# Optimization experiments

Hardware: AMD Instinct MI355X
Metric: run time of the kernel (lower is better)

## Reference

```python
import jax, jax.numpy as jnp
import numpy as np

D_MODEL, D_K, D_V, H = 1024, 64, 64, 16


def setup_inputs() -> dict:
    key = jax.random.key(0)
    ks = jax.random.split(key, 11)
    b, nq, nk = 2, 2048, 2048
    queries = jax.random.normal(ks[0], (b, nq, D_MODEL), dtype=jnp.float32)
    keys = jax.random.normal(ks[1], (b, nk, D_MODEL), dtype=jnp.float32)
    values = jax.random.normal(ks[2], (b, nk, D_MODEL), dtype=jnp.float32)
    def xavier(k, shape):
        fan_in, fan_out = shape[1], shape[0]
        lim = np.sqrt(6.0 / (fan_in + fan_out)).astype(np.float32)
        return jax.random.uniform(k, shape, jnp.float32, -lim, lim)
    # torch Linear weight shape: (out_features, in_features)
    Wq = xavier(ks[3], (H * D_K, D_MODEL)); bq = jnp.zeros((H * D_K,), jnp.float32)
    Wk = xavier(ks[4], (H * D_K, D_MODEL)); bk = jnp.zeros((H * D_K,), jnp.float32)
    Wv = xavier(ks[5], (H * D_V, D_MODEL)); bv = jnp.zeros((H * D_V,), jnp.float32)
    Wo = xavier(ks[6], (D_MODEL, H * D_V)); bo = jnp.zeros((D_MODEL,), jnp.float32)
    return {"queries": queries, "keys": keys, "values": values,
            "Wq": Wq, "bq": bq, "Wk": Wk, "bk": bk,
            "Wv": Wv, "bv": bv, "Wo": Wo, "bo": bo}


def reference(queries, keys, values, Wq, bq, Wk, bk, Wv, bv, Wo, bo):
    b, nq, _ = queries.shape
    nk = keys.shape[1]
    scale = 1.0 / np.sqrt(D_K).astype(np.float32)
    # projections -> (b, h, n, d)
    q = (queries @ Wq.T + bq).reshape(b, nq, H, D_K).transpose(0, 2, 1, 3)
    k = (keys @ Wk.T + bk).reshape(b, nk, H, D_K).transpose(0, 2, 1, 3)
    v = (values @ Wv.T + bv).reshape(b, nk, H, D_V).transpose(0, 2, 1, 3)
    att = jnp.einsum('bhqd,bhkd->bhqk', q, k) * scale  # (b,h,nq,nk)
    att = jax.nn.softmax(att, axis=-1)
    out = jnp.einsum('bhqk,bhkd->bhqd', att, v)        # (b,h,nq,dv)
    out = out.transpose(0, 2, 1, 3).reshape(b, nq, H * D_V)
    return out @ Wo.T + bo
```

## Files before the change

### kernel.cpp

```cpp
#include <hip/hip_runtime.h>
#include <stdint.h>

typedef __bf16 v8bf __attribute__((ext_vector_type(8)));
typedef float  v4f  __attribute__((ext_vector_type(4)));

#define QSCALE 0.18033688011112042f

typedef __attribute__((address_space(3))) void lds_vp;
typedef const __attribute__((address_space(1))) void gbl_vp;
__device__ __forceinline__ void gl_lds16(const __bf16* g, __bf16* l) {
    __builtin_amdgcn_global_load_lds((gbl_vp*)g, (lds_vp*)l, 16, 0, 0);
}

__device__ __forceinline__ v8bf cvt8(const float* __restrict__ p) {
    float4 x = *reinterpret_cast<const float4*>(p);
    float4 y = *reinterpret_cast<const float4*>(p + 4);
    v8bf r;
    r[0] = (__bf16)x.x; r[1] = (__bf16)x.y; r[2] = (__bf16)x.z; r[3] = (__bf16)x.w;
    r[4] = (__bf16)y.x; r[5] = (__bf16)y.y; r[6] = (__bf16)y.z; r[7] = (__bf16)y.w;
    return r;
}

__global__ __launch_bounds__(256) void cvt_w(
    const float* __restrict__ w0, const float* __restrict__ w1,
    const float* __restrict__ w2, const float* __restrict__ w3,
    __bf16* __restrict__ o0, __bf16* __restrict__ o1,
    __bf16* __restrict__ o2, __bf16* __restrict__ o3)
{
    const float* src; __bf16* dst;
    switch (blockIdx.y) {
        case 0: src = w0; dst = o0; break;
        case 1: src = w1; dst = o1; break;
        case 2: src = w2; dst = o2; break;
        default: src = w3; dst = o3; break;
    }
    size_t i = ((size_t)blockIdx.x * 256 + threadIdx.x) * 8;
    *reinterpret_cast<v8bf*>(dst + i) = cvt8(src + i);
}

__global__ __launch_bounds__(256) void cvt_in(
    const float* __restrict__ i0, const float* __restrict__ i1,
    const float* __restrict__ i2,
    __bf16* __restrict__ o0, __bf16* __restrict__ o1, __bf16* __restrict__ o2)
{
    const float* src; __bf16* dst;
    switch (blockIdx.y) {
        case 0: src = i0; dst = o0; break;
        case 1: src = i1; dst = o1; break;
        default: src = i2; dst = o2; break;
    }
    size_t i = ((size_t)blockIdx.x * 256 + threadIdx.x) * 8;
    *reinterpret_cast<v8bf*>(dst + i) = cvt8(src + i);
}

template<int MT>
__device__ __forceinline__ void gemm_body(
    const __bf16* __restrict__ A, const __bf16* __restrict__ W,
    const float* __restrict__ bias, void* __restrict__ outp,
    int mode, float oscale, int bx, int by)
{
    constexpr int K = 1024, N = 1024;
    constexpr int WM = MT / 32;
    constexpr int AI = MT / 32;
    constexpr int BI = 4;
    __shared__ __align__(16) __bf16 As[MT * 64];
    __shared__ __align__(16) __bf16 Bs[128 * 64];

    const int lane = threadIdx.x & 63;
    const int wave = threadIdx.x >> 6;
    const int quad = lane >> 4;
    const int l15  = lane & 15;
    const int m_base = bx * MT;
    const int n_base = by * 128;
    const int wm = (wave & 1) * (MT / 2);
    const int wn = (wave >> 1) * 64;

    int arow[AI], acol[AI], brow[BI], bcol[BI];
    #pragma unroll
    for (int i = 0; i < AI; ++i) {
        int L = (i * 4 + wave) * 64 + lane;
        int r = L >> 3, s = L & 7;
        arow[i] = r; acol[i] = (s ^ (r & 7)) * 8;
    }
    #pragma unroll
    for (int i = 0; i < BI; ++i) {
        int L = (i * 4 + wave) * 64 + lane;
        int r = L >> 3, s = L & 7;
        brow[i] = r; bcol[i] = (s ^ (r & 7)) * 8;
    }

    v4f acc[WM][4];
    #pragma unroll
    for (int fa = 0; fa < WM; ++fa)
        #pragma unroll
        for (int fb = 0; fb < 4; ++fb) { v4f z = {0.f,0.f,0.f,0.f}; acc[fa][fb] = z; }

    for (int kb = 0; kb < K; kb += 64) {
        #pragma unroll
        for (int i = 0; i < AI; ++i)
            gl_lds16(A + (size_t)(m_base + arow[i]) * K + kb + acol[i],
                     &As[(size_t)(i * 4 + wave) * 512]);
        #pragma unroll
        for (int i = 0; i < BI; ++i)
            gl_lds16(W + (size_t)(n_base + brow[i]) * K + kb + bcol[i],
                     &Bs[(size_t)(i * 4 + wave) * 512]);
        __syncthreads();
        #pragma unroll
        for (int ks = 0; ks < 2; ++ks) {
            v8bf af[WM], bf[4];
            #pragma unroll
            for (int f = 0; f < WM; ++f) {
                const int R = wm + f * 16 + l15;
                const int slot = (ks * 4 + quad) ^ (R & 7);
                af[f] = *reinterpret_cast<const v8bf*>(&As[R * 64 + slot * 8]);
            }
            #pragma unroll
            for (int f = 0; f < 4; ++f) {
                const int R = wn + f * 16 + l15;
                const int slot = (ks * 4 + quad) ^ (R & 7);
                bf[f] = *reinterpret_cast<const v8bf*>(&Bs[R * 64 + slot * 8]);
            }
            #pragma unroll
            for (int fa = 0; fa < WM; ++fa)
                #pragma unroll
                for (int fb = 0; fb < 4; ++fb)
                    acc[fa][fb] = __builtin_amdgcn_mfma_f32_16x16x32_bf16(
                        af[fa], bf[fb], acc[fa][fb], 0, 0, 0);
        }
        __syncthreads();
    }

    #pragma unroll
    for (int fa = 0; fa < WM; ++fa)
        #pragma unroll
        for (int fb = 0; fb < 4; ++fb) {
            const int nc = n_base + wn + fb * 16 + l15;
            const float bval = bias[nc];
            #pragma unroll
            for (int r = 0; r < 4; ++r) {
                const int m = m_base + wm + fa * 16 + quad * 4 + r;
                const float v = (acc[fa][fb][r] + bval) * oscale;
                if (mode == 2) {
                    ((float*)outp)[(size_t)m * N + nc] = v;
                } else {
                    int b = m >> 11, n = m & 2047, h = nc >> 6, d = nc & 63;
                    size_t off = (mode == 0)
                        ? ((size_t)(b * 16 + h) * 2048 + n) * 64 + d
                        : ((size_t)(b * 16 + h) * 64 + d) * 2048 + n;
                    ((__bf16*)outp)[off] = (__bf16)v;
                }
            }
        }
}

__global__ __launch_bounds__(256) void qkv_gemm(
    const __bf16* __restrict__ Aq, const __bf16* __restrict__ Ak,
    const __bf16* __restrict__ Av,
    const __bf16* __restrict__ Wq, const __bf16* __restrict__ Wk,
    const __bf16* __restrict__ Wv,
    const float* __restrict__ bq, const float* __restrict__ bk,
    const float* __restrict__ bv,
    __bf16* __restrict__ Qo, __bf16* __restrict__ Ko, __bf16* __restrict__ Vo)
{
    const __bf16 *A, *W; const float* bias; __bf16* outp; float oscale; int mode;
    switch (blockIdx.z) {
        case 0:  A = Aq; W = Wq; bias = bq; outp = Qo; oscale = QSCALE; mode = 0; break;
        case 1:  A = Ak; W = Wk; bias = bk; outp = Ko; oscale = 1.0f;   mode = 0; break;
        default: A = Av; W = Wv; bias = bv; outp = Vo; oscale = 1.0f;   mode = 1; break;
    }
    gemm_body<128>(A, W, bias, outp, mode, oscale, blockIdx.x, blockIdx.y);
}

__global__ __launch_bounds__(256) void out_gemm(
    const __bf16* __restrict__ A, const __bf16* __restrict__ W,
    const float* __restrict__ bias, float* __restrict__ outp)
{
    gemm_body<64>(A, W, bias, outp, 2, 1.0f, blockIdx.x, blockIdx.y);
}

__global__ __launch_bounds__(256) void attn_kernel(
    const __bf16* __restrict__ Q, const __bf16* __restrict__ Kb_,
    const __bf16* __restrict__ Vt, __bf16* __restrict__ O)
{
    __shared__ __align__(16) __bf16 Ks[64 * 64];
    __shared__ __align__(16) __bf16 Vs[64 * 64];
    __shared__ __align__(16) __bf16 p_lds[4][2][16][72];

    const int lane = threadIdx.x & 63;
    const int wave = threadIdx.x >> 6;
    const int quad = lane >> 4;
    const int l15  = lane & 15;
    const int qt = blockIdx.x;
    const int bh = blockIdx.y;
    const int b  = bh >> 4, h = bh & 15;

    const __bf16* Qh = Q   + (size_t)bh * 2048 * 64;
    const __bf16* Kh = Kb_ + (size_t)bh * 2048 * 64;
    const __bf16* Vh = Vt  + (size_t)bh * 64 * 2048;

    int srow[2], scol[2];
    #pragma unroll
    for (int i = 0; i < 2; ++i) {
        int L = (i * 4 + wave) * 64 + lane;
        int r = L >> 3, s = L & 7;
        srow[i] = r; scol[i] = (s ^ (r & 7)) * 8;
    }

    v8bf qf[2][2];
    #pragma unroll
    for (int s = 0; s < 2; ++s)
        #pragma unroll
        for (int ks = 0; ks < 2; ++ks)
            qf[s][ks] = *reinterpret_cast<const v8bf*>(
                Qh + (size_t)(qt * 128 + wave * 32 + s * 16 + l15) * 64 + ks * 32 + quad * 8);

    v4f o_acc[2][4];
    #pragma unroll
    for (int s = 0; s < 2; ++s)
        #pragma unroll
        for (int c = 0; c < 4; ++c) { v4f z = {0.f,0.f,0.f,0.f}; o_acc[s][c] = z; }
    float l_r[2][4];
    #pragma unroll
    for (int s = 0; s < 2; ++s)
        #pragma unroll
        for (int r = 0; r < 4; ++r) l_r[s][r] = 0.f;

    for (int kt = 0; kt < 32; ++kt) {
        #pragma unroll
        for (int i = 0; i < 2; ++i) {
            gl_lds16(Kh + (size_t)(kt * 64 + srow[i]) * 64 + scol[i],
                     &Ks[(size_t)(i * 4 + wave) * 512]);
            gl_lds16(Vh + (size_t)srow[i] * 2048 + kt * 64 + scol[i],
                     &Vs[(size_t)(i * 4 + wave) * 512]);
        }
        __syncthreads();

        v4f s_t[2][4];
        #pragma unroll
        for (int s = 0; s < 2; ++s)
            #pragma unroll
            for (int c = 0; c < 4; ++c) { v4f z = {0.f,0.f,0.f,0.f}; s_t[s][c] = z; }
        #pragma unroll
        for (int ks = 0; ks < 2; ++ks) {
            v8bf kf[4];
            #pragma unroll
            for (int c = 0; c < 4; ++c) {
                const int R = c * 16 + l15;
                const int slot = (ks * 4 + quad) ^ (R & 7);
                kf[c] = *reinterpret_cast<const v8bf*>(&Ks[R * 64 + slot * 8]);
            }
            #pragma unroll
            for (int c = 0; c < 4; ++c) {
                s_t[0][c] = __builtin_amdgcn_mfma_f32_16x16x32_bf16(qf[0][ks], kf[c], s_t[0][c], 0, 0, 0);
                s_t[1][c] = __builtin_amdgcn_mfma_f32_16x16x32_bf16(qf[1][ks], kf[c], s_t[1][c], 0, 0, 0);
            }
        }

        #pragma unroll
        for (int s = 0; s < 2; ++s)
            #pragma unroll
            for (int r = 0; r < 4; ++r) {
                const float p0 = __builtin_exp2f(s_t[s][0][r]);
                const float p1 = __builtin_exp2f(s_t[s][1][r]);
                const float p2 = __builtin_exp2f(s_t[s][2][r]);
                const float p3 = __builtin_exp2f(s_t[s][3][r]);
                l_r[s][r] += (p0 + p1) + (p2 + p3);
                p_lds[wave][s][quad * 4 + r][0 * 16 + l15] = (__bf16)p0;
                p_lds[wave][s][quad * 4 + r][1 * 16 + l15] = (__bf16)p1;
                p_lds[wave][s][quad * 4 + r][2 * 16 + l15] = (__bf16)p2;
                p_lds[wave][s][quad * 4 + r][3 * 16 + l15] = (__bf16)p3;
            }

        #pragma unroll
        for (int ks = 0; ks < 2; ++ks) {
            v8bf vf[4];
            #pragma unroll
            for (int c = 0; c < 4; ++c) {
                const int R = c * 16 + l15;
                const int slot = (ks * 4 + quad) ^ (R & 7);
                vf[c] = *reinterpret_cast<const v8bf*>(&Vs[R * 64 + slot * 8]);
            }
            #pragma unroll
            for (int s = 0; s < 2; ++s) {
                v8bf pf = *reinterpret_cast<const v8bf*>(&p_lds[wave][s][l15][ks * 32 + quad * 8]);
                #pragma unroll
                for (int c = 0; c < 4; ++c)
                    o_acc[s][c] = __builtin_amdgcn_mfma_f32_16x16x32_bf16(pf, vf[c], o_acc[s][c], 0, 0, 0);
            }
        }
        __syncthreads();
    }

    #pragma unroll
    for (int s = 0; s < 2; ++s)
        #pragma unroll
        for (int r = 0; r < 4; ++r) {
            float l = l_r[s][r];
            #pragma unroll
            for (int off = 1; off < 16; off <<= 1)
                l += __shfl_xor(l, off, 16);
            const float inv_l = 1.0f / l;
            const int qr = qt * 128 + wave * 32 + s * 16 + quad * 4 + r;
            #pragma unroll
            for (int c = 0; c < 4; ++c) {
                const int col = h * 64 + c * 16 + l15;
                O[(size_t)(b * 2048 + qr) * 1024 + col] = (__bf16)(o_acc[s][c][r] * inv_l);
            }
        }
}

extern "C" void kernel_launch(void* const* d_in, const int* in_sizes, int n_in,
                              void* d_out, int out_size, void* d_ws, size_t ws_size,
                              hipStream_t stream) {
    const float* q_in = (const float*)d_in[0];
    const float* k_in = (const float*)d_in[1];
    const float* v_in = (const float*)d_in[2];
    const float* Wq = (const float*)d_in[3];
    const float* bq = (const float*)d_in[4];
    const float* Wk = (const float*)d_in[5];
    const float* bk = (const float*)d_in[6];
    const float* Wv = (const float*)d_in[7];
    const float* bv = (const float*)d_in[8];
    const float* Wo = (const float*)d_in[9];
    const float* bo = (const float*)d_in[10];
    float* out = (float*)d_out;

    __bf16* ws  = (__bf16*)d_ws;
    __bf16* Abq = ws;
    __bf16* Abk = Abq + 4194304;
    __bf16* Abv = Abk + 4194304;
    __bf16* Qb  = Abv + 4194304;
    __bf16* Kb  = Qb  + 4194304;
    __bf16* Vb  = Kb  + 4194304;
    __bf16* Wqb = Vb  + 4194304;
    __bf16* Wkb = Wqb + 1048576;
    __bf16* Wvb = Wkb + 1048576;
    __bf16* Wob = Wvb + 1048576;
    __bf16* Ob  = Abq;

    cvt_w<<<dim3(512, 4), 256, 0, stream>>>(Wq, Wk, Wv, Wo, Wqb, Wkb, Wvb, Wob);
    cvt_in<<<dim3(2048, 3), 256, 0, stream>>>(q_in, k_in, v_in, Abq, Abk, Abv);

    qkv_gemm<<<dim3(32, 8, 3), 256, 0, stream>>>(
        Abq, Abk, Abv, Wqb, Wkb, Wvb, bq, bk, bv, Qb, Kb, Vb);

    attn_kernel<<<dim3(16, 32), 256, 0, stream>>>(Qb, Kb, Vb, Ob);

    out_gemm<<<dim3(64, 8), 256, 0, stream>>>(Ob, Wob, bo, out);
}
```

Baseline: 255.5 us.

## Double-buffer LDS tiles in GEMMs and attention, retile and remap block order

Result: no change. 254.7 us (-0.3%).

```diff
diff --git a/kernel.cpp b/kernel.cpp
--- a/kernel.cpp
+++ b/kernel.cpp
@@ -53,93 +53,101 @@
     *reinterpret_cast<v8bf*>(dst + i) = cvt8(src + i);
 }
 
-template<int MT>
 __device__ __forceinline__ void gemm_body(
     const __bf16* __restrict__ A, const __bf16* __restrict__ W,
     const float* __restrict__ bias, void* __restrict__ outp,
     int mode, float oscale, int bx, int by)
 {
     constexpr int K = 1024, N = 1024;
-    constexpr int WM = MT / 32;
-    constexpr int AI = MT / 32;
-    constexpr int BI = 4;
-    __shared__ __align__(16) __bf16 As[MT * 64];
-    __shared__ __align__(16) __bf16 Bs[128 * 64];
+    __shared__ __align__(16) __bf16 As[2][128 * 64];
+    __shared__ __align__(16) __bf16 Bs[2][64 * 64];
 
     const int lane = threadIdx.x & 63;
     const int wave = threadIdx.x >> 6;
     const int quad = lane >> 4;
     const int l15  = lane & 15;
-    const int m_base = bx * MT;
-    const int n_base = by * 128;
-    const int wm = (wave & 1) * (MT / 2);
-    const int wn = (wave >> 1) * 64;
-
-    int arow[AI], acol[AI], brow[BI], bcol[BI];
-    #pragma unroll
-    for (int i = 0; i < AI; ++i) {
+    const int m_base = bx * 128;
+    const int n_base = by * 64;
+    const int wm = (wave & 1) * 64;
+    const int wn = (wave >> 1) * 32;
+
+    int arow[4], acol[4], brow[2], bcol[2];
+    #pragma unroll
+    for (int i = 0; i < 4; ++i) {
         int L = (i * 4 + wave) * 64 + lane;
         int r = L >> 3, s = L & 7;
         arow[i] = r; acol[i] = (s ^ (r & 7)) * 8;
     }
     #pragma unroll
-    for (int i = 0; i < BI; ++i) {
+    for (int i = 0; i < 2; ++i) {
         int L = (i * 4 + wave) * 64 + lane;
         int r = L >> 3, s = L & 7;
         brow[i] = r; bcol[i] = (s ^ (r & 7)) * 8;
     }
 
-    v4f acc[WM][4];
-    #pragma unroll
-    for (int fa = 0; fa < WM; ++fa)
-        #pragma unroll
-        for (int fb = 0; fb < 4; ++fb) { v4f z = {0.f,0.f,0.f,0.f}; acc[fa][fb] = z; }
-
-    for (int kb = 0; kb < K; kb += 64) {
-        #pragma unroll
-        for (int i = 0; i < AI; ++i)
-            gl_lds16(A + (size_t)(m_base + arow[i]) * K + kb + acol[i],
-                     &As[(size_t)(i * 4 + wave) * 512]);
-        #pragma unroll
-        for (int i = 0; i < BI; ++i)
-            gl_lds16(W + (size_t)(n_base + brow[i]) * K + kb + bcol[i],
-                     &Bs[(size_t)(i * 4 + wave) * 512]);
-        __syncthreads();
+    v4f acc[4][2];
+    #pragma unroll
+    for (int f = 0; f < 4; ++f)
+        #pragma unroll
+        for (int g = 0; g < 2; ++g) { v4f z = {0.f,0.f,0.f,0.f}; acc[f][g] = z; }
+
+    #pragma unroll
+    for (int i = 0; i < 4; ++i)
+        gl_lds16(A + (size_t)(m_base + arow[i]) * K + acol[i],
+                 &As[0][(i * 4 + wave) * 512]);
+    #pragma unroll
+    for (int i = 0; i < 2; ++i)
+        gl_lds16(W + (size_t)(n_base + brow[i]) * K + bcol[i],
+                 &Bs[0][(i * 4 + wave) * 512]);
+    __syncthreads();
+
+    for (int it = 0; it < 16; ++it) {
+        const int cur = it & 1, nxt = cur ^ 1;
+        const int kn = ((it + 1) & 15) * 64;
+        #pragma unroll
+        for (int i = 0; i < 4; ++i)
+            gl_lds16(A + (size_t)(m_base + arow[i]) * K + kn + acol[i],
+                     &As[nxt][(i * 4 + wave) * 512]);
+        #pragma unroll
+        for (int i = 0; i < 2; ++i)
+            gl_lds16(W + (size_t)(n_base + brow[i]) * K + kn + bcol[i],
+                     &Bs[nxt][(i * 4 + wave) * 512]);
+
         #pragma unroll
         for (int ks = 0; ks < 2; ++ks) {
-            v8bf af[WM], bf[4];
-            #pragma unroll
-            for (int f = 0; f < WM; ++f) {
+            v8bf af[4], bf[2];
+            #pragma unroll
+            for (int f = 0; f < 4; ++f) {
                 const int R = wm + f * 16 + l15;
                 const int slot = (ks * 4 + quad) ^ (R & 7);
-                af[f] = *reinterpret_cast<const v8bf*>(&As[R * 64 + slot * 8]);
-            }
-            #pragma unroll
-            for (int f = 0; f < 4; ++f) {
-                const int R = wn + f * 16 + l15;
+                af[f] = *reinterpret_cast<const v8bf*>(&As[cur][R * 64 + slot * 8]);
+            }
+            #pragma unroll
+            for (int g = 0; g < 2; ++g) {
+                const int R = wn + g * 16 + l15;
                 const int slot = (ks * 4 + quad) ^ (R & 7);
-                bf[f] = *reinterpret_cast<const v8bf*>(&Bs[R * 64 + slot * 8]);
-            }
-            #pragma unroll
-            for (int fa = 0; fa < WM; ++fa)
+                bf[g] = *reinterpret_cast<const v8bf*>(&Bs[cur][R * 64 + slot * 8]);
+            }
+            #pragma unroll
+            for (int f = 0; f < 4; ++f)
                 #pragma unroll
-                for (int fb = 0; fb < 4; ++fb)
-                    acc[fa][fb] = __builtin_amdgcn_mfma_f32_16x16x32_bf16(
-                        af[fa], bf[fb], acc[fa][fb], 0, 0, 0);
+                for (int g = 0; g < 2; ++g)
+                    acc[f][g] = __builtin_amdgcn_mfma_f32_16x16x32_bf16(
+                        af[f], bf[g], acc[f][g], 0, 0, 0);
         }
         __syncthreads();
     }
 
     #pragma unroll
-    for (int fa = 0; fa < WM; ++fa)
-        #pragma unroll
-        for (int fb = 0; fb < 4; ++fb) {
-            const int nc = n_base + wn + fb * 16 + l15;
+    for (int f = 0; f < 4; ++f)
+        #pragma unroll
+        for (int g = 0; g < 2; ++g) {
+            const int nc = n_base + wn + g * 16 + l15;
             const float bval = bias[nc];
             #pragma unroll
             for (int r = 0; r < 4; ++r) {
-                const int m = m_base + wm + fa * 16 + quad * 4 + r;
-                const float v = (acc[fa][fb][r] + bval) * oscale;
+                const int m = m_base + wm + f * 16 + quad * 4 + r;
+                const float v = (acc[f][g][r] + bval) * oscale;
                 if (mode == 2) {
                     ((float*)outp)[(size_t)m * N + nc] = v;
                 } else {
@@ -162,36 +170,43 @@
     const float* __restrict__ bv,
     __bf16* __restrict__ Qo, __bf16* __restrict__ Ko, __bf16* __restrict__ Vo)
 {
+    const int id = blockIdx.x;
+    const int by = id & 15;
+    const int bx = (id >> 4) & 31;
+    const int z  = id >> 9;
+
     const __bf16 *A, *W; const float* bias; __bf16* outp; float oscale; int mode;
-    switch (blockIdx.z) {
+    switch (z) {
         case 0:  A = Aq; W = Wq; bias = bq; outp = Qo; oscale = QSCALE; mode = 0; break;
         case 1:  A = Ak; W = Wk; bias = bk; outp = Ko; oscale = 1.0f;   mode = 0; break;
         default: A = Av; W = Wv; bias = bv; outp = Vo; oscale = 1.0f;   mode = 1; break;
     }
-    gemm_body<128>(A, W, bias, outp, mode, oscale, blockIdx.x, blockIdx.y);
+    gemm_body(A, W, bias, outp, mode, oscale, bx, by);
 }
 
 __global__ __launch_bounds__(256) void out_gemm(
     const __bf16* __restrict__ A, const __bf16* __restrict__ W,
     const float* __restrict__ bias, float* __restrict__ outp)
 {
-    gemm_body<64>(A, W, bias, outp, 2, 1.0f, blockIdx.x, blockIdx.y);
+    const int by = blockIdx.x & 15;
+    const int bx = blockIdx.x >> 4;
+    gemm_body(A, W, bias, outp, 2, 1.0f, bx, by);
 }
 
 __global__ __launch_bounds__(256) void attn_kernel(
     const __bf16* __restrict__ Q, const __bf16* __restrict__ Kb_,
     const __bf16* __restrict__ Vt, __bf16* __restrict__ O)
 {
-    __shared__ __align__(16) __bf16 Ks[64 * 64];
-    __shared__ __align__(16) __bf16 Vs[64 * 64];
+    __shared__ __align__(16) __bf16 Ks[2][64 * 64];
+    __shared__ __align__(16) __bf16 Vs[2][64 * 64];
     __shared__ __align__(16) __bf16 p_lds[4][2][16][72];
 
     const int lane = threadIdx.x & 63;
     const int wave = threadIdx.x >> 6;
     const int quad = lane >> 4;
     const int l15  = lane & 15;
-    const int qt = blockIdx.x;
-    const int bh = blockIdx.y;
+    const int bh = blockIdx.x & 31;
+    const int qt = blockIdx.x >> 5;
     const int b  = bh >> 4, h = bh & 15;
 
     const __bf16* Qh = Q   + (size_t)bh * 2048 * 64;
@@ -225,15 +240,23 @@
         #pragma unroll
         for (int r = 0; r < 4; ++r) l_r[s][r] = 0.f;
 
+    #pragma unroll
+    for (int i = 0; i < 2; ++i) {
+        gl_lds16(Kh + (size_t)srow[i] * 64 + scol[i], &Ks[0][(i * 4 + wave) * 512]);
+        gl_lds16(Vh + (size_t)srow[i] * 2048 + scol[i], &Vs[0][(i * 4 + wave) * 512]);
+    }
+    __syncthreads();
+
     for (int kt = 0; kt < 32; ++kt) {
+        const int cur = kt & 1, nxt = cur ^ 1;
+        const int ktn = (kt + 1) & 31;
         #pragma unroll
         for (int i = 0; i < 2; ++i) {
-            gl_lds16(Kh + (size_t)(kt * 64 + srow[i]) * 64 + scol[i],
-                     &Ks[(size_t)(i * 4 + wave) * 512]);
-            gl_lds16(Vh + (size_t)srow[i] * 2048 + kt * 64 + scol[i],
-                     &Vs[(size_t)(i * 4 + wave) * 512]);
-        }
-        __syncthreads();
+            gl_lds16(Kh + (size_t)(ktn * 64 + srow[i]) * 64 + scol[i],
+                     &Ks[nxt][(i * 4 + wave) * 512]);
+            gl_lds16(Vh + (size_t)srow[i] * 2048 + ktn * 64 + scol[i],
+                     &Vs[nxt][(i * 4 + wave) * 512]);
+        }
 
         v4f s_t[2][4];
         #pragma unroll
@@ -247,7 +270,7 @@
             for (int c = 0; c < 4; ++c) {
                 const int R = c * 16 + l15;
                 const int slot = (ks * 4 + quad) ^ (R & 7);
-                kf[c] = *reinterpret_cast<const v8bf*>(&Ks[R * 64 + slot * 8]);
+                kf[c] = *reinterpret_cast<const v8bf*>(&Ks[cur][R * 64 + slot * 8]);
             }
             #pragma unroll
             for (int c = 0; c < 4; ++c) {
@@ -278,7 +301,7 @@
             for (int c = 0; c < 4; ++c) {
                 const int R = c * 16 + l15;
                 const int slot = (ks * 4 + quad) ^ (R & 7);
-                vf[c] = *reinterpret_cast<const v8bf*>(&Vs[R * 64 + slot * 8]);
+                vf[c] = *reinterpret_cast<const v8bf*>(&Vs[cur][R * 64 + slot * 8]);
             }
             #pragma unroll
             for (int s = 0; s < 2; ++s) {
@@ -341,10 +364,10 @@
     cvt_w<<<dim3(512, 4), 256, 0, stream>>>(Wq, Wk, Wv, Wo, Wqb, Wkb, Wvb, Wob);
     cvt_in<<<dim3(2048, 3), 256, 0, stream>>>(q_in, k_in, v_in, Abq, Abk, Abv);
 
-    qkv_gemm<<<dim3(32, 8, 3), 256, 0, stream>>>(
+    qkv_gemm<<<1536, 256, 0, stream>>>(
         Abq, Abk, Abv, Wqb, Wkb, Wvb, bq, bk, bv, Qb, Kb, Vb);
 
-    attn_kernel<<<dim3(16, 32), 256, 0, stream>>>(Qb, Kb, Vb, Ob);
-
-    out_gemm<<<dim3(64, 8), 256, 0, stream>>>(Ob, Wob, bo, out);
-}
+    attn_kernel<<<512, 256, 0, stream>>>(Qb, Kb, Vb, Ob);
+
+    out_gemm<<<512, 256, 0, stream>>>(Ob, Wob, bo, out);
+}
```
